# Optimization experiments

Hardware: AMD Instinct MI355X
Metric: run time of the kernel (lower is better)

The kernel has to match this reference:

```python
import jax, jax.numpy as jnp
import numpy as np
from jax import lax

H = W = 496
K = 5            # gabor kernel size
WIN = 16         # window_size
STRIDE = 16
PATCH = 32
GAMMA = 0.5
PSI = np.pi / 2
THETAS = np.array([np.pi/8, np.pi/4, 3*np.pi/8, np.pi/2, 5*np.pi/8, 6*np.pi/8, 7*np.pi/8, np.pi], dtype=np.float32)


def setup_inputs() -> dict:
    key = jax.random.key(0)
    k1, k2, k3 = jax.random.split(key, 3)
    img = jax.random.normal(k1, (1, 1, H, W), dtype=jnp.float32)
    sigmas = jax.random.uniform(k2, (1, 3), dtype=jnp.float32) * 10.0   # nn.Parameter(rand*10)
    lambdas = jax.random.uniform(k3, (1, 3), dtype=jnp.float32) * np.pi  # nn.Parameter(rand*pi)
    return {"img": img, "sigmas": sigmas, "lambdas": lambdas}


def _gabor_bank(sigmas, lambdas):
    # axes: (sigma, lambda, theta, ky, kx)
    idx = jnp.arange(K, dtype=jnp.float32) - (K - 1) / 2.0
    sig = sigmas[0][:, None, None, None, None]          # [3,1,1,1,1]
    lam = lambdas[0][None, :, None, None, None]         # [1,3,1,1,1]
    th = jnp.asarray(THETAS)[None, None, :, None, None] # [1,1,8,1,1]
    y = idx[None, None, None, :, None]
    x = idx[None, None, None, None, :]
    sigma_x = sig
    sigma_y = sig / GAMMA
    sin_t, cos_t = jnp.sin(th), jnp.cos(th)
    y_theta = -x * sin_t + y * cos_t
    x_theta = x * cos_t + y * sin_t
    gb = jnp.exp(-0.5 * (x_theta**2 / sigma_x**2 + y_theta**2 / sigma_y**2)) \
         * jnp.cos(2.0 * np.pi * x_theta / lam + PSI)
    return gb.reshape(-1, 1, K, K)  # [72,1,5,5]


def reference(img, sigmas, lambdas):
    gb = _gabor_bank(sigmas, lambdas)
    res = lax.conv_general_dilated(
        img, gb, window_strides=(1, 1), padding=[(K // 2, K // 2)] * 2,
        dimension_numbers=("NCHW", "OIHW", "NCHW"))          # [1,72,H,W]
    res = res.reshape(1, 9, 8, H, W).max(axis=2)              # max over 8 thetas -> [1,9,H,W]
    out = res[0]                                              # [9,H,W]

    # find_maxima: per-channel threshold at 5*mean, zero below (torch.nn.Threshold)
    mean = out.mean(axis=(1, 2), keepdims=True)
    thr = jnp.where(out > mean * 5.0, out, 0.0)

    nw = H // STRIDE                                          # 31
    windows = thr.reshape(9, nw, WIN, nw, WIN).transpose(0, 1, 3, 2, 4).reshape(9, nw * nw, WIN * WIN)
    is_max = jnp.argmax(windows, axis=2) == (WIN * WIN) // 2  # [9, 961]

    w_idx = jnp.arange(nw * nw)
    rows = w_idx // nw * STRIDE + WIN // 2
    cols = w_idx % nw * STRIDE + WIN // 2

    # describe: zero-pad by 16, gather 32x32 patch at each candidate keypoint for every channel
    pad = jnp.pad(out, ((0, 0), (16, 16), (16, 16)))
    pr = rows[:, None, None] + jnp.arange(PATCH)[None, :, None]   # [961,32,1]
    pc = cols[:, None, None] + jnp.arange(PATCH)[None, None, :]   # [961,1,32]
    patches = pad[:, pr, pc]                                      # [9,961,32,32]

    # keep patches only for detected keypoints with nonzero content (original skips zero patches)
    valid_kp = jnp.any(is_max, axis=0)                            # [961]
    nonzero = jnp.any(patches != 0, axis=(2, 3))                  # [9,961]
    mask = (valid_kp[None, :] & nonzero).astype(patches.dtype)
    patches = patches * mask[:, :, None, None]
    return patches
```

## Files before the change

kernel.cpp:

```cpp
#include <hip/hip_runtime.h>
#include <math.h>

#define HH 496
#define WW 496
#define HWSZ (HH*WW)
#define NW 31
#define NWIN (NW*NW)
#define PARTSTRIDE 1024

typedef float nf4 __attribute__((ext_vector_type(4)));

__constant__ float c_thetas[8] = {
    0.39269908169872414f, 0.7853981633974483f, 1.1780972450961724f,
    1.5707963267948966f,  1.9634954084936207f, 2.356194490192345f,
    2.748893571891069f,   3.141592653589793f};

#define FMAS(B, P) \
    a0  = fmaf(P, flds[(B)+0],  a0);  a1  = fmaf(P, flds[(B)+1],  a1);  \
    a2  = fmaf(P, flds[(B)+2],  a2);  a3  = fmaf(P, flds[(B)+3],  a3);  \
    a4  = fmaf(P, flds[(B)+4],  a4);  a5  = fmaf(P, flds[(B)+5],  a5);  \
    a6  = fmaf(P, flds[(B)+6],  a6);  a7  = fmaf(P, flds[(B)+7],  a7);  \
    a8  = fmaf(P, flds[(B)+8],  a8);  a9  = fmaf(P, flds[(B)+9],  a9);  \
    a10 = fmaf(P, flds[(B)+10], a10); a11 = fmaf(P, flds[(B)+11], a11); \
    a12 = fmaf(P, flds[(B)+12], a12); a13 = fmaf(P, flds[(B)+13], a13); \
    a14 = fmaf(P, flds[(B)+14], a14); a15 = fmaf(P, flds[(B)+15], a15); \
    a16 = fmaf(P, flds[(B)+16], a16); a17 = fmaf(P, flds[(B)+17], a17); \
    a18 = fmaf(P, flds[(B)+18], a18); a19 = fmaf(P, flds[(B)+19], a19); \
    a20 = fmaf(P, flds[(B)+20], a20); a21 = fmaf(P, flds[(B)+21], a21); \
    a22 = fmaf(P, flds[(B)+22], a22); a23 = fmaf(P, flds[(B)+23], a23);

#define STEP(K, CG) { FMAS((K)*72 + (CG)*24, p##K) }

#define ALLSTEPS(CG) \
    STEP(0,CG)  STEP(1,CG)  STEP(2,CG)  STEP(3,CG)  STEP(4,CG)  \
    STEP(5,CG)  STEP(6,CG)  STEP(7,CG)  STEP(8,CG)  STEP(9,CG)  \
    STEP(10,CG) STEP(11,CG) STEP(12,CG) STEP(13,CG) STEP(14,CG) \
    STEP(15,CG) STEP(16,CG) STEP(17,CG) STEP(18,CG) STEP(19,CG) \
    STEP(20,CG) STEP(21,CG) STEP(22,CG) STEP(23,CG) STEP(24,CG)

#define RED(CC, MV) { \
        float s = MV; \
        s += __shfl_down(s, 32, 64); s += __shfl_down(s, 16, 64); \
        s += __shfl_down(s,  8, 64); s += __shfl_down(s,  4, 64); \
        s += __shfl_down(s,  2, 64); s += __shfl_down(s,  1, 64); \
        if ((tid & 63) == 0) red[tid >> 6][CC] = s; }

#define CONVCG(CG) { \
        float a0=0,a1=0,a2=0,a3=0,a4=0,a5=0,a6=0,a7=0,a8=0,a9=0,a10=0,a11=0, \
              a12=0,a13=0,a14=0,a15=0,a16=0,a17=0,a18=0,a19=0,a20=0,a21=0,a22=0,a23=0; \
        ALLSTEPS(CG) \
        float m0 = fmaxf(fmaxf(fmaxf(a0,a1),fmaxf(a2,a3)),fmaxf(fmaxf(a4,a5),fmaxf(a6,a7))); \
        float m1 = fmaxf(fmaxf(fmaxf(a8,a9),fmaxf(a10,a11)),fmaxf(fmaxf(a12,a13),fmaxf(a14,a15))); \
        float m2 = fmaxf(fmaxf(fmaxf(a16,a17),fmaxf(a18,a19)),fmaxf(fmaxf(a20,a21),fmaxf(a22,a23))); \
        out[((CG) * 3 + 0) * HWSZ + y * WW + x] = m0; \
        out[((CG) * 3 + 1) * HWSZ + y * WW + x] = m1; \
        out[((CG) * 3 + 2) * HWSZ + y * WW + x] = m2; \
        RED((CG) * 3 + 0, m0) RED((CG) * 3 + 1, m1) RED((CG) * 3 + 2, m2) \
    }

__global__ __launch_bounds__(256) void conv_kernel(
    const float* __restrict__ img,
    const float* __restrict__ sigmas, const float* __restrict__ lambdas,
    float* __restrict__ out, float* __restrict__ partial) {
    __shared__ float tile[20 * 20];
    __shared__ __align__(16) float flds[1800];
    __shared__ float red[4][9];
    int tid = threadIdx.x;
    int tx = tid & 15, ty = tid >> 4;
    int bx = blockIdx.x, by = blockIdx.y;

    for (int i = tid; i < 400; i += 256) {
        int tY = i / 20, tX = i % 20;
        int gy = by * 16 + tY - 2, gx = bx * 16 + tX - 2;
        float v = 0.0f;
        if (gy >= 0 && gy < HH && gx >= 0 && gx < WW) v = img[gy * WW + gx];
        tile[i] = v;
    }
    for (int idx = tid; idx < 1800; idx += 256) {
        int f = idx / 25, k = idx % 25;
        int dy = k / 5, dx = k % 5;
        int s = f / 24, rem = f % 24, l = rem / 8, t = rem % 8;
        float sig = sigmas[s], lam = lambdas[l], th = c_thetas[t];
        float yy = (float)dy - 2.0f, xx = (float)dx - 2.0f;
        float st = sinf(th), ct = cosf(th);
        float yt = -xx * st + yy * ct;
        float xt =  xx * ct + yy * st;
        float sx2 = sig * sig;
        float sy2 = 4.0f * sig * sig;
        float g = expf(-0.5f * (xt * xt / sx2 + yt * yt / sy2)) *
                  cosf(6.28318530717958647692f * xt / lam + 1.5707963267948966f);
        flds[k * 72 + f] = g;
    }
    __syncthreads();

    int tbase = ty * 20 + tx;
    float p0  = tile[tbase +  0], p1  = tile[tbase +  1], p2  = tile[tbase +  2],
          p3  = tile[tbase +  3], p4  = tile[tbase +  4];
    float p5  = tile[tbase + 20], p6  = tile[tbase + 21], p7  = tile[tbase + 22],
          p8  = tile[tbase + 23], p9  = tile[tbase + 24];
    float p10 = tile[tbase + 40], p11 = tile[tbase + 41], p12 = tile[tbase + 42],
          p13 = tile[tbase + 43], p14 = tile[tbase + 44];
    float p15 = tile[tbase + 60], p16 = tile[tbase + 61], p17 = tile[tbase + 62],
          p18 = tile[tbase + 63], p19 = tile[tbase + 64];
    float p20 = tile[tbase + 80], p21 = tile[tbase + 81], p22 = tile[tbase + 82],
          p23 = tile[tbase + 83], p24 = tile[tbase + 84];

    int y = by * 16 + ty, x = bx * 16 + tx;

    CONVCG(0)
    CONVCG(1)
    CONVCG(2)

    __syncthreads();
    if (tid < 9) {
        int bid = by * NW + bx;
        partial[tid * PARTSTRIDE + bid] =
            red[0][tid] + red[1][tid] + red[2][tid] + red[3][tid];
    }
}

__global__ __launch_bounds__(256) void patch_kernel(
    const float* __restrict__ out, const float* __restrict__ partial,
    float* __restrict__ dst) {
    int w = blockIdx.x;
    int r = w / NW, cl = w % NW;
    int tid = threadIdx.x;
    __shared__ float sm5[9];
    __shared__ int lds_and[4];
    __shared__ int lds_or[4];

    {
        int lane = tid & 63, wid = tid >> 6;
        for (int c = wid; c < 9; c += 4) {
            float s = 0.0f;
            for (int b = lane; b < NWIN; b += 64) s += partial[c * PARTSTRIDE + b];
            s += __shfl_down(s, 32, 64); s += __shfl_down(s, 16, 64);
            s += __shfl_down(s,  8, 64); s += __shfl_down(s,  4, 64);
            s += __shfl_down(s,  2, 64); s += __shfl_down(s,  1, 64);
            if (lane == 0) sm5[c] = s * (5.0f / (float)HWSZ);
        }
    }
    __syncthreads();

    int wy = tid >> 4, wx = tid & 15;
    int rowbase = (r * 16 + wy) * WW + cl * 16 + wx;
    int cbase   = (r * 16 + 8) * WW + cl * 16;
    int okmask = 0;
#pragma unroll
    for (int c = 0; c < 9; c++) {
        float m5 = sm5[c];
        float v  = out[c * HWSZ + rowbase];
        float vc = out[c * HWSZ + cbase];
        float thr  = (v  > m5) ? v  : 0.0f;
        float thrc = (vc > m5) ? vc : 0.0f;
        bool ok = (tid < 128) ? (thr < thrc) : (thr <= thrc);
        okmask |= (ok ? 1 : 0) << c;
    }
#pragma unroll
    for (int off = 1; off < 64; off <<= 1) okmask &= __shfl_xor(okmask, off, 64);
    if ((tid & 63) == 0) lds_and[tid >> 6] = okmask;
    __syncthreads();

    int am = lds_and[0] & lds_and[1] & lds_and[2] & lds_and[3];

    int i = tid >> 3;
    int jg = (tid & 7) << 2;
    size_t dbase = (size_t)w * 1024 + i * 32 + jg;

    if (am == 0) {
        nf4 z = (nf4){0.f, 0.f, 0.f, 0.f};
#pragma unroll
        for (int c = 0; c < 9; c++)
            __builtin_nontemporal_store(z, (nf4*)(dst + (size_t)c * NWIN * 1024 + dbase));
        return;
    }

    int row = r * 16 + i - 8;
    int col = cl * 16 + jg - 8;
    bool inb = (row >= 0 && row < HH && col >= 0 && col + 3 < WW);
    size_t pbase = (size_t)row * WW + col;
    int nzmask = 0;
    nf4 p0, p1, p2, p3, p4, p5, p6, p7, p8;
#define LOADP(C, V) { \
        V = (nf4){0.f, 0.f, 0.f, 0.f}; \
        if (inb) V = *(const nf4*)(out + (size_t)(C) * HWSZ + pbase); \
        if (V.x != 0.f || V.y != 0.f || V.z != 0.f || V.w != 0.f) nzmask |= 1 << (C); }
    LOADP(0,p0) LOADP(1,p1) LOADP(2,p2) LOADP(3,p3) LOADP(4,p4)
    LOADP(5,p5) LOADP(6,p6) LOADP(7,p7) LOADP(8,p8)

#pragma unroll
    for (int off = 1; off < 64; off <<= 1) nzmask |= __shfl_xor(nzmask, off, 64);
    if ((tid & 63) == 0) lds_or[tid >> 6] = nzmask;
    __syncthreads();

    int om = lds_or[0] | lds_or[1] | lds_or[2] | lds_or[3];

#define STOREP(C, V) { \
        float mk = ((om >> (C)) & 1) ? 1.0f : 0.0f; \
        V *= mk; \
        __builtin_nontemporal_store(V, (nf4*)(dst + (size_t)(C) * NWIN * 1024 + dbase)); }
    STOREP(0,p0) STOREP(1,p1) STOREP(2,p2) STOREP(3,p3) STOREP(4,p4)
    STOREP(5,p5) STOREP(6,p6) STOREP(7,p7) STOREP(8,p8)
}

extern "C" void kernel_launch(void* const* d_in, const int* in_sizes, int n_in,
                              void* d_out, int out_size, void* d_ws, size_t ws_size,
                              hipStream_t stream) {
    const float* img     = (const float*)d_in[0];
    const float* sigmas  = (const float*)d_in[1];
    const float* lambdas = (const float*)d_in[2];
    float* ws = (float*)d_ws;
    float* partial = ws;
    float* outb    = ws + 16384;

    conv_kernel<<<dim3(NW, NW), 256, 0, stream>>>(img, sigmas, lambdas, outb, partial);
    patch_kernel<<<NWIN, 256, 0, stream>>>(outb, partial, (float*)d_out);
}
```

Baseline: 119.0 us.

## Register-block convolution to 2x2 outputs per thread with 32x32 block tiles

Each thread now computes a 2x2 group of output pixels, so every filter weight read from shared memory feeds four FMAs instead of one. Blocks cover 32x32 pixels with a 36x36 halo tile, which cuts the grid to 16x16 blocks and reduces redundant Gabor-bank construction per block. The channel-group loop is kept rolled, and launch bounds request one block per SM to leave room for about 96 accumulators plus 36 input registers per thread. The tradeoffs are far fewer blocks (256) on a large GPU, lower occupancy, and edge blocks that are only partly used.

```diff
diff --git a/kernel.cpp b/kernel.cpp
--- a/kernel.cpp
+++ b/kernel.cpp
@@ -6,72 +6,68 @@
 #define HWSZ (HH*WW)
 #define NW 31
 #define NWIN (NW*NW)
+#define NB 16
+#define NCONVB (NB*NB)
 #define PARTSTRIDE 1024
 
 typedef float nf4 __attribute__((ext_vector_type(4)));
+typedef float nf2 __attribute__((ext_vector_type(2)));
 
 __constant__ float c_thetas[8] = {
     0.39269908169872414f, 0.7853981633974483f, 1.1780972450961724f,
     1.5707963267948966f,  1.9634954084936207f, 2.356194490192345f,
     2.748893571891069f,   3.141592653589793f};
 
-#define FMAS(B, P) \
-    a0  = fmaf(P, flds[(B)+0],  a0);  a1  = fmaf(P, flds[(B)+1],  a1);  \
-    a2  = fmaf(P, flds[(B)+2],  a2);  a3  = fmaf(P, flds[(B)+3],  a3);  \
-    a4  = fmaf(P, flds[(B)+4],  a4);  a5  = fmaf(P, flds[(B)+5],  a5);  \
-    a6  = fmaf(P, flds[(B)+6],  a6);  a7  = fmaf(P, flds[(B)+7],  a7);  \
-    a8  = fmaf(P, flds[(B)+8],  a8);  a9  = fmaf(P, flds[(B)+9],  a9);  \
-    a10 = fmaf(P, flds[(B)+10], a10); a11 = fmaf(P, flds[(B)+11], a11); \
-    a12 = fmaf(P, flds[(B)+12], a12); a13 = fmaf(P, flds[(B)+13], a13); \
-    a14 = fmaf(P, flds[(B)+14], a14); a15 = fmaf(P, flds[(B)+15], a15); \
-    a16 = fmaf(P, flds[(B)+16], a16); a17 = fmaf(P, flds[(B)+17], a17); \
-    a18 = fmaf(P, flds[(B)+18], a18); a19 = fmaf(P, flds[(B)+19], a19); \
-    a20 = fmaf(P, flds[(B)+20], a20); a21 = fmaf(P, flds[(B)+21], a21); \
-    a22 = fmaf(P, flds[(B)+22], a22); a23 = fmaf(P, flds[(B)+23], a23);
-
-#define STEP(K, CG) { FMAS((K)*72 + (CG)*24, p##K) }
-
-#define ALLSTEPS(CG) \
-    STEP(0,CG)  STEP(1,CG)  STEP(2,CG)  STEP(3,CG)  STEP(4,CG)  \
-    STEP(5,CG)  STEP(6,CG)  STEP(7,CG)  STEP(8,CG)  STEP(9,CG)  \
-    STEP(10,CG) STEP(11,CG) STEP(12,CG) STEP(13,CG) STEP(14,CG) \
-    STEP(15,CG) STEP(16,CG) STEP(17,CG) STEP(18,CG) STEP(19,CG) \
-    STEP(20,CG) STEP(21,CG) STEP(22,CG) STEP(23,CG) STEP(24,CG)
+
+#define F4(N, PA, PB, PC, PD) { float w = flds[fb + (N)]; \
+    q##N = fmaf(PA, w, q##N); r##N = fmaf(PB, w, r##N); \
+    s##N = fmaf(PC, w, s##N); t##N = fmaf(PD, w, t##N); }
+
+#define STEP(K, PA, PB, PC, PD) { const int fb = cgo + (K)*72; \
+    F4(0,PA,PB,PC,PD)  F4(1,PA,PB,PC,PD)  F4(2,PA,PB,PC,PD)  F4(3,PA,PB,PC,PD)  \
+    F4(4,PA,PB,PC,PD)  F4(5,PA,PB,PC,PD)  F4(6,PA,PB,PC,PD)  F4(7,PA,PB,PC,PD)  \
+    F4(8,PA,PB,PC,PD)  F4(9,PA,PB,PC,PD)  F4(10,PA,PB,PC,PD) F4(11,PA,PB,PC,PD) \
+    F4(12,PA,PB,PC,PD) F4(13,PA,PB,PC,PD) F4(14,PA,PB,PC,PD) F4(15,PA,PB,PC,PD) \
+    F4(16,PA,PB,PC,PD) F4(17,PA,PB,PC,PD) F4(18,PA,PB,PC,PD) F4(19,PA,PB,PC,PD) \
+    F4(20,PA,PB,PC,PD) F4(21,PA,PB,PC,PD) F4(22,PA,PB,PC,PD) F4(23,PA,PB,PC,PD) }
+
+#define ALLSTEPS \
+    STEP(0,  p00,p01,p10,p11) STEP(1,  p01,p02,p11,p12) STEP(2,  p02,p03,p12,p13) \
+    STEP(3,  p03,p04,p13,p14) STEP(4,  p04,p05,p14,p15) \
+    STEP(5,  p10,p11,p20,p21) STEP(6,  p11,p12,p21,p22) STEP(7,  p12,p13,p22,p23) \
+    STEP(8,  p13,p14,p23,p24) STEP(9,  p14,p15,p24,p25) \
+    STEP(10, p20,p21,p30,p31) STEP(11, p21,p22,p31,p32) STEP(12, p22,p23,p32,p33) \
+    STEP(13, p23,p24,p33,p34) STEP(14, p24,p25,p34,p35) \
+    STEP(15, p30,p31,p40,p41) STEP(16, p31,p32,p41,p42) STEP(17, p32,p33,p42,p43) \
+    STEP(18, p33,p34,p43,p44) STEP(19, p34,p35,p44,p45) \
+    STEP(20, p40,p41,p50,p51) STEP(21, p41,p42,p51,p52) STEP(22, p42,p43,p52,p53) \
+    STEP(23, p43,p44,p53,p54) STEP(24, p44,p45,p54,p55)
+
+#define MAX8(A,B,C,D,E,F,G,H) \
+    fmaxf(fmaxf(fmaxf(A,B),fmaxf(C,D)),fmaxf(fmaxf(E,F),fmaxf(G,H)))
 
 #define RED(CC, MV) { \
-        float s = MV; \
-        s += __shfl_down(s, 32, 64); s += __shfl_down(s, 16, 64); \
-        s += __shfl_down(s,  8, 64); s += __shfl_down(s,  4, 64); \
-        s += __shfl_down(s,  2, 64); s += __shfl_down(s,  1, 64); \
-        if ((tid & 63) == 0) red[tid >> 6][CC] = s; }
-
-#define CONVCG(CG) { \
-        float a0=0,a1=0,a2=0,a3=0,a4=0,a5=0,a6=0,a7=0,a8=0,a9=0,a10=0,a11=0, \
-              a12=0,a13=0,a14=0,a15=0,a16=0,a17=0,a18=0,a19=0,a20=0,a21=0,a22=0,a23=0; \
-        ALLSTEPS(CG) \
-        float m0 = fmaxf(fmaxf(fmaxf(a0,a1),fmaxf(a2,a3)),fmaxf(fmaxf(a4,a5),fmaxf(a6,a7))); \
-        float m1 = fmaxf(fmaxf(fmaxf(a8,a9),fmaxf(a10,a11)),fmaxf(fmaxf(a12,a13),fmaxf(a14,a15))); \
-        float m2 = fmaxf(fmaxf(fmaxf(a16,a17),fmaxf(a18,a19)),fmaxf(fmaxf(a20,a21),fmaxf(a22,a23))); \
-        out[((CG) * 3 + 0) * HWSZ + y * WW + x] = m0; \
-        out[((CG) * 3 + 1) * HWSZ + y * WW + x] = m1; \
-        out[((CG) * 3 + 2) * HWSZ + y * WW + x] = m2; \
-        RED((CG) * 3 + 0, m0) RED((CG) * 3 + 1, m1) RED((CG) * 3 + 2, m2) \
-    }
-
-__global__ __launch_bounds__(256) void conv_kernel(
+        float s_ = MV; \
+        s_ += __shfl_down(s_, 32, 64); s_ += __shfl_down(s_, 16, 64); \
+        s_ += __shfl_down(s_,  8, 64); s_ += __shfl_down(s_,  4, 64); \
+        s_ += __shfl_down(s_,  2, 64); s_ += __shfl_down(s_,  1, 64); \
+        if ((tid & 63) == 0) red[tid >> 6][CC] = s_; }
+
+__global__ __launch_bounds__(256, 1) void conv_kernel(
     const float* __restrict__ img,
     const float* __restrict__ sigmas, const float* __restrict__ lambdas,
     float* __restrict__ out, float* __restrict__ partial) {
-    __shared__ float tile[20 * 20];
+    __shared__ float tile[36 * 36];
     __shared__ __align__(16) float flds[1800];
     __shared__ float red[4][9];
     int tid = threadIdx.x;
     int tx = tid & 15, ty = tid >> 4;
     int bx = blockIdx.x, by = blockIdx.y;
-
-    for (int i = tid; i < 400; i += 256) {
-        int tY = i / 20, tX = i % 20;
-        int gy = by * 16 + tY - 2, gx = bx * 16 + tX - 2;
+    int x0 = bx * 32, y0 = by * 32;
+
+    for (int i = tid; i < 1296; i += 256) {
+        int tY = i / 36, tX = i % 36;
+        int gy = y0 + tY - 2, gx = x0 + tX - 2;
         float v = 0.0f;
         if (gy >= 0 && gy < HH && gx >= 0 && gx < WW) v = img[gy * WW + gx];
         tile[i] = v;
@@ -93,27 +89,57 @@
     }
     __syncthreads();
 
-    int tbase = ty * 20 + tx;
-    float p0  = tile[tbase +  0], p1  = tile[tbase +  1], p2  = tile[tbase +  2],
-          p3  = tile[tbase +  3], p4  = tile[tbase +  4];
-    float p5  = tile[tbase + 20], p6  = tile[tbase + 21], p7  = tile[tbase + 22],
-          p8  = tile[tbase + 23], p9  = tile[tbase + 24];
-    float p10 = tile[tbase + 40], p11 = tile[tbase + 41], p12 = tile[tbase + 42],
-          p13 = tile[tbase + 43], p14 = tile[tbase + 44];
-    float p15 = tile[tbase + 60], p16 = tile[tbase + 61], p17 = tile[tbase + 62],
-          p18 = tile[tbase + 63], p19 = tile[tbase + 64];
-    float p20 = tile[tbase + 80], p21 = tile[tbase + 81], p22 = tile[tbase + 82],
-          p23 = tile[tbase + 83], p24 = tile[tbase + 84];
-
-    int y = by * 16 + ty, x = bx * 16 + tx;
-
-    CONVCG(0)
-    CONVCG(1)
-    CONVCG(2)
+    int rb = (2 * ty) * 36 + 2 * tx;
+    float p00=tile[rb+  0], p01=tile[rb+  1], p02=tile[rb+  2], p03=tile[rb+  3], p04=tile[rb+  4], p05=tile[rb+  5];
+    float p10=tile[rb+ 36], p11=tile[rb+ 37], p12=tile[rb+ 38], p13=tile[rb+ 39], p14=tile[rb+ 40], p15=tile[rb+ 41];
+    float p20=tile[rb+ 72], p21=tile[rb+ 73], p22=tile[rb+ 74], p23=tile[rb+ 75], p24=tile[rb+ 76], p25=tile[rb+ 77];
+    float p30=tile[rb+108], p31=tile[rb+109], p32=tile[rb+110], p33=tile[rb+111], p34=tile[rb+112], p35=tile[rb+113];
+    float p40=tile[rb+144], p41=tile[rb+145], p42=tile[rb+146], p43=tile[rb+147], p44=tile[rb+148], p45=tile[rb+149];
+    float p50=tile[rb+180], p51=tile[rb+181], p52=tile[rb+182], p53=tile[rb+183], p54=tile[rb+184], p55=tile[rb+185];
+
+    int xx0 = x0 + 2 * tx, yy0 = y0 + 2 * ty;
+    bool inb = (xx0 < WW) && (yy0 < HH);
+
+#pragma unroll 1
+    for (int cg = 0; cg < 3; ++cg) {
+        const int cgo = cg * 24;
+        float q0=0,q1=0,q2=0,q3=0,q4=0,q5=0,q6=0,q7=0,q8=0,q9=0,q10=0,q11=0,
+              q12=0,q13=0,q14=0,q15=0,q16=0,q17=0,q18=0,q19=0,q20=0,q21=0,q22=0,q23=0;
+        float r0=0,r1=0,r2=0,r3=0,r4=0,r5=0,r6=0,r7=0,r8=0,r9=0,r10=0,r11=0,
+              r12=0,r13=0,r14=0,r15=0,r16=0,r17=0,r18=0,r19=0,r20=0,r21=0,r22=0,r23=0;
+        float s0=0,s1=0,s2=0,s3=0,s4=0,s5=0,s6=0,s7=0,s8=0,s9=0,s10=0,s11=0,
+              s12=0,s13=0,s14=0,s15=0,s16=0,s17=0,s18=0,s19=0,s20=0,s21=0,s22=0,s23=0;
+        float t0=0,t1=0,t2=0,t3=0,t4=0,t5=0,t6=0,t7=0,t8=0,t9=0,t10=0,t11=0,
+              t12=0,t13=0,t14=0,t15=0,t16=0,t17=0,t18=0,t19=0,t20=0,t21=0,t22=0,t23=0;
+
+        ALLSTEPS
+
+        float mq0=MAX8(q0,q1,q2,q3,q4,q5,q6,q7),     mq1=MAX8(q8,q9,q10,q11,q12,q13,q14,q15),
+              mq2=MAX8(q16,q17,q18,q19,q20,q21,q22,q23);
+        float mr0=MAX8(r0,r1,r2,r3,r4,r5,r6,r7),     mr1=MAX8(r8,r9,r10,r11,r12,r13,r14,r15),
+              mr2=MAX8(r16,r17,r18,r19,r20,r21,r22,r23);
+        float ms0=MAX8(s0,s1,s2,s3,s4,s5,s6,s7),     ms1=MAX8(s8,s9,s10,s11,s12,s13,s14,s15),
+              ms2=MAX8(s16,s17,s18,s19,s20,s21,s22,s23);
+        float mt0=MAX8(t0,t1,t2,t3,t4,t5,t6,t7),     mt1=MAX8(t8,t9,t10,t11,t12,t13,t14,t15),
+              mt2=MAX8(t16,t17,t18,t19,t20,t21,t22,t23);
+
+#define EPI(J, MQ, MR, MS, MT) { \
+            int ch = cg * 3 + (J); \
+            if (inb) { \
+                *(nf2*)(out + (size_t)ch * HWSZ + (size_t)yy0 * WW + xx0)       = (nf2){MQ, MR}; \
+                *(nf2*)(out + (size_t)ch * HWSZ + (size_t)(yy0 + 1) * WW + xx0) = (nf2){MS, MT}; \
+            } \
+            float sm = inb ? (MQ + MR + MS + MT) : 0.0f; \
+            RED(ch, sm) }
+        EPI(0, mq0, mr0, ms0, mt0)
+        EPI(1, mq1, mr1, ms1, mt1)
+        EPI(2, mq2, mr2, ms2, mt2)
+#undef EPI
+    }
 
     __syncthreads();
     if (tid < 9) {
-        int bid = by * NW + bx;
+        int bid = by * NB + bx;
         partial[tid * PARTSTRIDE + bid] =
             red[0][tid] + red[1][tid] + red[2][tid] + red[3][tid];
     }
@@ -133,7 +159,7 @@
         int lane = tid & 63, wid = tid >> 6;
         for (int c = wid; c < 9; c += 4) {
             float s = 0.0f;
-            for (int b = lane; b < NWIN; b += 64) s += partial[c * PARTSTRIDE + b];
+            for (int b = lane; b < NCONVB; b += 64) s += partial[c * PARTSTRIDE + b];
             s += __shfl_down(s, 32, 64); s += __shfl_down(s, 16, 64);
             s += __shfl_down(s,  8, 64); s += __shfl_down(s,  4, 64);
             s += __shfl_down(s,  2, 64); s += __shfl_down(s,  1, 64);
@@ -213,6 +239,6 @@
     float* partial = ws;
     float* outb    = ws + 16384;
 
-    conv_kernel<<<dim3(NW, NW), 256, 0, stream>>>(img, sigmas, lambdas, outb, partial);
+    conv_kernel<<<dim3(NB, NB), 256, 0, stream>>>(img, sigmas, lambdas, outb, partial);
     patch_kernel<<<NWIN, 256, 0, stream>>>(outb, partial, (float*)d_out);
 }
```

Result: slower. 149.6 us (+25.7%).
